# Performance work log

Hardware: AMD Instinct MI355X
Metric: run time of the kernel (lower is better)

The kernel has to match this reference:

```python
import jax, jax.numpy as jnp
import numpy as np

N_HEAD = 16

def setup_inputs() -> dict:
    key = jax.random.key(0)
    ks = jax.random.split(key, 9)
    B, T, C = 4, 2048, 1024
    s = 1.0 / np.sqrt(C)
    return {
        "x":  jax.random.normal(ks[0], (B, T, C), jnp.float32),
        "Wq": jax.random.normal(ks[1], (C, C), jnp.float32) * s,
        "bq": jax.random.normal(ks[2], (C,), jnp.float32) * 0.02,
        "Wk": jax.random.normal(ks[3], (C, C), jnp.float32) * s,
        "bk": jax.random.normal(ks[4], (C,), jnp.float32) * 0.02,
        "Wv": jax.random.normal(ks[5], (C, C), jnp.float32) * s,
        "bv": jax.random.normal(ks[6], (C,), jnp.float32) * 0.02,
        "Wp": jax.random.normal(ks[7], (C, C), jnp.float32) * s,
        "bp": jax.random.normal(ks[8], (C,), jnp.float32) * 0.02,
    }

def reference(x, Wq, bq, Wk, bk, Wv, bv, Wp, bp):
    B, T, C = x.shape
    H, D = N_HEAD, C // N_HEAD
    # torch nn.Linear: y = x @ W^T + b
    q = (x @ Wq.T + bq).reshape(B, T, H, D).transpose(0, 2, 1, 3)  # [B,H,T,D]
    k = (x @ Wk.T + bk).reshape(B, T, H, D).transpose(0, 2, 1, 3)
    v = (x @ Wv.T + bv).reshape(B, T, H, D).transpose(0, 2, 1, 3)
    # full TxT causal attention (non-flash path)
    att = jnp.einsum('bhtd,bhsd->bhts', q, k) * (1.0 / np.sqrt(D))  # [B,H,T,T]
    causal = jnp.tril(jnp.ones((T, T), dtype=bool))
    att = jnp.where(causal[None, None], att, -jnp.inf)
    att = jax.nn.softmax(att, axis=-1)
    y = jnp.einsum('bhts,bhsd->bhtd', att, v)  # [B,H,T,D]
    y = y.transpose(0, 2, 1, 3).reshape(B, T, C)
    return y @ Wp.T + bp
```

## Files before the change

### kernel.cpp

```cpp
#include <hip/hip_runtime.h>

typedef __bf16 bf16_t;
typedef __bf16 bf16x8 __attribute__((ext_vector_type(8)));
typedef __bf16 bf16x4 __attribute__((ext_vector_type(4)));
typedef float f32x4 __attribute__((ext_vector_type(4)));
typedef unsigned short ushort_t;

#define T_SEQ 2048
#define C_DIM 1024
#define NH    16
#define HD    64

__device__ __forceinline__ ushort_t f2bf(float f) {
    unsigned u = __builtin_bit_cast(unsigned, f);
    u += 0x7FFFu + ((u >> 16) & 1u);
    return (ushort_t)(u >> 16);
}

__device__ __forceinline__ void async_cp16(const void* g, void* l) {
    __builtin_amdgcn_global_load_lds(
        (const __attribute__((address_space(1))) void*)g,
        (__attribute__((address_space(3))) void*)l, 16, 0, 0);
}

#define X4  2097152
#define W4  262144
__global__ __launch_bounds__(256)
void cvt_all_kernel(const float* __restrict__ x,  const float* __restrict__ Wq,
                    const float* __restrict__ Wk, const float* __restrict__ Wv,
                    ushort_t* __restrict__ xb,  ushort_t* __restrict__ Wqb,
                    ushort_t* __restrict__ Wkb, ushort_t* __restrict__ Wvb) {
    int i = blockIdx.x * 256 + threadIdx.x;
    const float* src; ushort_t* dst; int off;
    if (i < X4)                { src = x;  dst = xb;  off = i; }
    else if (i < X4 + W4)      { src = Wq; dst = Wqb; off = i - X4; }
    else if (i < X4 + 2 * W4)  { src = Wk; dst = Wkb; off = i - X4 - W4; }
    else                       { src = Wv; dst = Wvb; off = i - X4 - 2 * W4; }
    float4 f = ((const float4*)src)[off];
    ushort4 u;
    u.x = f2bf(f.x); u.y = f2bf(f.y); u.z = f2bf(f.z); u.w = f2bf(f.w);
    ((ushort4*)dst)[off] = u;
}

__global__ __launch_bounds__(256)
void cvt_wp_kernel(const float* __restrict__ Wp, ushort_t* __restrict__ Wpb) {
    int i = blockIdx.x * 256 + threadIdx.x;
    float4 f = ((const float4*)Wp)[i];
    ushort4 u;
    u.x = f2bf(f.x); u.y = f2bf(f.y); u.z = f2bf(f.z); u.w = f2bf(f.w);
    ((ushort4*)Wpb)[i] = u;
}

__device__ __forceinline__ void gemm_core_128(const bf16_t* __restrict__ A,
                                              const bf16_t* __restrict__ B,
                                              f32x4 (&acc)[4][4]) {
    __shared__ alignas(16) ushort_t As[128 * 64];
    __shared__ alignas(16) ushort_t Ws[128 * 64];
    const int tid  = threadIdx.x;
    const int lane = tid & 63;
    const int wv   = tid >> 6;
    const int wm   = wv >> 1, wn = wv & 1;
    const int quad = lane >> 4, ln = lane & 15;
    const int m0 = blockIdx.x * 128, n0 = blockIdx.y * 128;

    f32x4 z4 = {0.f, 0.f, 0.f, 0.f};
#pragma unroll
    for (int i = 0; i < 4; i++)
#pragma unroll
        for (int j = 0; j < 4; j++) acc[i][j] = z4;

    const int lr = lane >> 3;
    const int lc = (lane & 7) ^ lr;
    const bf16_t* Ab = A + (size_t)(m0 + wv * 32 + lr) * 1024 + lc * 8;
    const bf16_t* Bb = B + (size_t)(n0 + wv * 32 + lr) * 1024 + lc * 8;

    for (int kt = 0; kt < 1024; kt += 64) {
#pragma unroll
        for (int p = 0; p < 4; ++p) {
            async_cp16(Ab + (size_t)p * 8192 + kt, &As[(wv * 4 + p) * 512]);
            async_cp16(Bb + (size_t)p * 8192 + kt, &Ws[(wv * 4 + p) * 512]);
        }
        __syncthreads();
#pragma unroll
        for (int ks = 0; ks < 2; ++ks) {
            bf16x8 af[4], bfr[4];
#pragma unroll
            for (int i = 0; i < 4; i++)
                af[i] = *(const bf16x8*)&As[(wm * 64 + i * 16 + ln) * 64 +
                                            (((ks * 4 + quad) ^ (ln & 7)) * 8)];
#pragma unroll
            for (int j = 0; j < 4; j++)
                bfr[j] = *(const bf16x8*)&Ws[(wn * 64 + j * 16 + ln) * 64 +
                                             (((ks * 4 + quad) ^ (ln & 7)) * 8)];
#pragma unroll
            for (int i = 0; i < 4; i++)
#pragma unroll
                for (int j = 0; j < 4; j++)
                    acc[i][j] = __builtin_amdgcn_mfma_f32_16x16x32_bf16(af[i], bfr[j],
                                                                        acc[i][j], 0, 0, 0);
        }
        __syncthreads();
    }
}

__global__ __launch_bounds__(256, 3)
void qkv_gemm_kernel(const bf16_t* __restrict__ xb,
                     const bf16_t* __restrict__ Wqb, const float* __restrict__ bq,
                     const bf16_t* __restrict__ Wkb, const float* __restrict__ bk,
                     const bf16_t* __restrict__ Wvb, const float* __restrict__ bv,
                     ushort_t* __restrict__ Qo, ushort_t* __restrict__ Ko,
                     ushort_t* __restrict__ Vo) {
    const int z = blockIdx.z;
    const bf16_t* W   = (z == 0) ? Wqb : (z == 1) ? Wkb : Wvb;
    const float* bias = (z == 0) ? bq : (z == 1) ? bk : bv;
    ushort_t* outp    = (z == 0) ? Qo : (z == 1) ? Ko : Vo;
    const float fs    = (z == 0) ? 0.18033688011112042f : 1.0f;

    f32x4 acc[4][4];
    gemm_core_128(xb, W, acc);

    const int tid  = threadIdx.x;
    const int lane = tid & 63;
    const int wv2  = tid >> 6;
    const int wm   = wv2 >> 1, wn = wv2 & 1;
    const int quad = lane >> 4, ln = lane & 15;
    const int mbase = blockIdx.x * 128 + wm * 64;
    const int nbase = blockIdx.y * 128 + wn * 64;

#pragma unroll
    for (int j = 0; j < 4; j++) {
        int n = nbase + j * 16 + ln;
        float bj = bias[n];
        int h = n >> 6, d = n & 63;
#pragma unroll
        for (int i = 0; i < 4; i++) {
            int mr = mbase + i * 16 + quad * 4;
            int b = mr >> 11;
            int t = mr & 2047;
            if (z < 2) {
                ushort_t* op = outp + ((size_t)(b * NH + h) * T_SEQ + t) * HD + d;
#pragma unroll
                for (int r = 0; r < 4; r++)
                    op[(size_t)r * HD] = f2bf((acc[i][j][r] + bj) * fs);
            } else {
                ushort4 us;
                us.x = f2bf(acc[i][j][0] + bj);
                us.y = f2bf(acc[i][j][1] + bj);
                us.z = f2bf(acc[i][j][2] + bj);
                us.w = f2bf(acc[i][j][3] + bj);
                *(ushort4*)(outp + ((size_t)(b * NH + h) * HD + d) * T_SEQ + t) = us;
            }
        }
    }
}

__device__ __forceinline__ void qk2_softmax(const ushort_t* __restrict__ Ks,
                                            bf16_t* __restrict__ PsWA,
                                            bf16_t* __restrict__ PsWB,
                                            bf16x8 aqA0, bf16x8 aqA1,
                                            bf16x8 aqB0, bf16x8 aqB1,
                                            bool doA, bool diagA, bool diagB,
                                            int wv, int quad, int ln) {
#pragma unroll
    for (int n16 = 0; n16 < 4; n16++) {
        bf16x8 bk0 = *(const bf16x8*)&Ks[(n16 * 16 + ln) * 72 + quad * 8];
        bf16x8 bk1 = *(const bf16x8*)&Ks[(n16 * 16 + ln) * 72 + 32 + quad * 8];
        f32x4 zB = {0.f, 0.f, 0.f, 0.f};
        zB = __builtin_amdgcn_mfma_f32_16x16x32_bf16(bk0, aqB0, zB, 0, 0, 0);
        zB = __builtin_amdgcn_mfma_f32_16x16x32_bf16(bk1, aqB1, zB, 0, 0, 0);
        if (doA) {
            f32x4 zA = {0.f, 0.f, 0.f, 0.f};
            zA = __builtin_amdgcn_mfma_f32_16x16x32_bf16(bk0, aqA0, zA, 0, 0, 0);
            zA = __builtin_amdgcn_mfma_f32_16x16x32_bf16(bk1, aqA1, zA, 0, 0, 0);
            bf16x4 pa;
#pragma unroll
            for (int r = 0; r < 4; r++) {
                float v = zA[r];
                v = (diagA && (n16 * 16 + quad * 4 + r > wv * 16 + ln)) ? -1e30f : v;
                pa[r] = (bf16_t)__builtin_amdgcn_exp2f(v);
            }
            *(bf16x4*)&PsWA[ln * 72 + n16 * 16 + quad * 4] = pa;
        }
        bf16x4 pb;
#pragma unroll
        for (int r = 0; r < 4; r++) {
            float v = zB[r];
            v = (diagB && (n16 * 16 + quad * 4 + r > wv * 16 + ln)) ? -1e30f : v;
            pb[r] = (bf16_t)__builtin_amdgcn_exp2f(v);
        }
        *(bf16x4*)&PsWB[ln * 72 + n16 * 16 + quad * 4] = pb;
    }
}

__global__ __launch_bounds__(256, 4)
void flash_kernel(const ushort_t* __restrict__ Qw, const ushort_t* __restrict__ Kw,
                  const ushort_t* __restrict__ Vt, ushort_t* __restrict__ Y) {
    __shared__ alignas(16) ushort_t Ks[64 * 72];
    __shared__ alignas(16) ushort_t Vts[64 * 72];
    __shared__ alignas(16) bf16_t PsA[4 * 16 * 72];
    __shared__ alignas(16) bf16_t PsB[4 * 16 * 72];

    const int tid  = threadIdx.x;
    const int lane = tid & 63;
    const int wv   = tid >> 6;
    const int quad = lane >> 4, ln = lane & 15;
    const int L  = blockIdx.y * 16 + blockIdx.x;
    const int m  = L >> 3;
    const int bh = ((m >> 4) << 3) | (L & 7);
    const int p  = m & 15;
    const int qa = p, qb = 31 - p;
    const int b = bh >> 4, h = bh & 15;
    bf16_t* PsWA = &PsA[wv * 1152];
    bf16_t* PsWB = &PsB[wv * 1152];

    bf16x8 ones;
#pragma unroll
    for (int i = 0; i < 8; i++) ones[i] = (bf16_t)1.0f;

    const ushort_t* qpa = Qw + ((size_t)bh * T_SEQ + qa * 64 + wv * 16 + ln) * HD;
    const ushort_t* qpb = Qw + ((size_t)bh * T_SEQ + qb * 64 + wv * 16 + ln) * HD;
    bf16x8 aqA0 = *(const bf16x8*)(qpa + quad * 8);
    bf16x8 aqA1 = *(const bf16x8*)(qpa + 32 + quad * 8);
    bf16x8 aqB0 = *(const bf16x8*)(qpb + quad * 8);
    bf16x8 aqB1 = *(const bf16x8*)(qpb + 32 + quad * 8);

    f32x4 oA[4], oB[4];
    f32x4 z4 = {0.f, 0.f, 0.f, 0.f};
#pragma unroll
    for (int i = 0; i < 4; i++) { oA[i] = z4; oB[i] = z4; }
    f32x4 lA4 = z4, lB4 = z4;

    const int row0 = tid >> 3, c80 = (tid & 7) * 8;
    const int row1 = (256 + tid) >> 3, c81 = c80;

    uint4 pk0, pk1, pv0, pv1;
    pk0 = *(const uint4*)(Kw + ((size_t)bh * T_SEQ + row0) * HD + c80);
    pv0 = *(const uint4*)(Vt + ((size_t)bh * HD + row0) * T_SEQ + c80);
    pk1 = *(const uint4*)(Kw + ((size_t)bh * T_SEQ + row1) * HD + c81);
    pv1 = *(const uint4*)(Vt + ((size_t)bh * HD + row1) * T_SEQ + c81);

    for (int st = 0; st <= qb; ++st) {
        __syncthreads();
        *(uint4*)&Ks[row0 * 72 + c80]  = pk0;
        *(uint4*)&Vts[row0 * 72 + c80] = pv0;
        *(uint4*)&Ks[row1 * 72 + c81]  = pk1;
        *(uint4*)&Vts[row1 * 72 + c81] = pv1;
        if (st < qb) {
            int s1 = (st + 1) * 64;
            pk0 = *(const uint4*)(Kw + ((size_t)bh * T_SEQ + s1 + row0) * HD + c80);
            pv0 = *(const uint4*)(Vt + ((size_t)bh * HD + row0) * T_SEQ + s1 + c80);
            pk1 = *(const uint4*)(Kw + ((size_t)bh * T_SEQ + s1 + row1) * HD + c81);
            pv1 = *(const uint4*)(Vt + ((size_t)bh * HD + row1) * T_SEQ + s1 + c81);
        }
        __syncthreads();

        const bool doA = (st <= qa);
        qk2_softmax(Ks, PsWA, PsWB, aqA0, aqA1, aqB0, aqB1,
                    doA, st == qa, st == qb, wv, quad, ln);

#pragma unroll
        for (int ks = 0; ks < 2; ks++) {
            bf16x8 apA, apB;
            if (doA) {
                apA = *(const bf16x8*)&PsWA[ln * 72 + ks * 32 + quad * 8];
                lA4 = __builtin_amdgcn_mfma_f32_16x16x32_bf16(apA, ones, lA4, 0, 0, 0);
            }
            apB = *(const bf16x8*)&PsWB[ln * 72 + ks * 32 + quad * 8];
            lB4 = __builtin_amdgcn_mfma_f32_16x16x32_bf16(apB, ones, lB4, 0, 0, 0);
#pragma unroll
            for (int d16 = 0; d16 < 4; d16++) {
                bf16x8 bv = *(const bf16x8*)&Vts[(d16 * 16 + ln) * 72 + ks * 32 + quad * 8];
                if (doA)
                    oA[d16] = __builtin_amdgcn_mfma_f32_16x16x32_bf16(apA, bv, oA[d16], 0, 0, 0);
                oB[d16] = __builtin_amdgcn_mfma_f32_16x16x32_bf16(apB, bv, oB[d16], 0, 0, 0);
            }
        }
    }

#pragma unroll
    for (int ph = 0; ph < 2; ph++) {
        f32x4* o = ph ? oB : oA;
        f32x4 l4 = ph ? lB4 : lA4;
        int qt = ph ? qb : qa;
        f32x4 inv = {1.f / l4[0], 1.f / l4[1], 1.f / l4[2], 1.f / l4[3]};
        const int tg = qt * 64 + wv * 16 + quad * 4;
#pragma unroll
        for (int d16 = 0; d16 < 4; d16++) {
#pragma unroll
            for (int r = 0; r < 4; r++) {
                float v = o[d16][r] * inv[r];
                Y[((size_t)b * T_SEQ + tg + r) * C_DIM + h * HD + d16 * 16 + ln] = f2bf(v);
            }
        }
    }
}

__global__ __launch_bounds__(256, 3)
void proj_gemm_kernel(const bf16_t* __restrict__ Yw, const bf16_t* __restrict__ Wpb,
                      const float* __restrict__ bp, float* __restrict__ out) {
    f32x4 acc[4][4];
    gemm_core_128(Yw, Wpb, acc);

    const int tid  = threadIdx.x;
    const int lane = tid & 63;
    const int wv2  = tid >> 6;
    const int wm   = wv2 >> 1, wn = wv2 & 1;
    const int quad = lane >> 4, ln = lane & 15;
    const int mbase = blockIdx.x * 128 + wm * 64;
    const int nbase = blockIdx.y * 128 + wn * 64;

#pragma unroll
    for (int j = 0; j < 4; j++) {
        int n = nbase + j * 16 + ln;
        float bj = bp[n];
#pragma unroll
        for (int i = 0; i < 4; i++) {
            int mr = mbase + i * 16 + quad * 4;
#pragma unroll
            for (int r = 0; r < 4; r++)
                out[(size_t)(mr + r) * C_DIM + n] = acc[i][j][r] + bj;
        }
    }
}

extern "C" void kernel_launch(void* const* d_in, const int* in_sizes, int n_in,
                              void* d_out, int out_size, void* d_ws, size_t ws_size,
                              hipStream_t stream) {
    const float* x  = (const float*)d_in[0];
    const float* Wq = (const float*)d_in[1];
    const float* bq = (const float*)d_in[2];
    const float* Wk = (const float*)d_in[3];
    const float* bk = (const float*)d_in[4];
    const float* Wv = (const float*)d_in[5];
    const float* bv = (const float*)d_in[6];
    const float* Wp = (const float*)d_in[7];
    const float* bp = (const float*)d_in[8];
    float* out = (float*)d_out;

    char* ws = (char*)d_ws;
    const size_t MB = (size_t)1 << 20;
    ushort_t* Qw = (ushort_t*)(ws);
    ushort_t* Kw = (ushort_t*)(ws + 16 * MB);
    ushort_t* Vt = (ushort_t*)(ws + 32 * MB);
    ushort_t* Yw = (ushort_t*)(ws + 48 * MB);
    ushort_t* Wpb = (ushort_t*)(ws);

    ushort_t* xb  = (ushort_t*)out;
    ushort_t* Wqb = (ushort_t*)((char*)out + 16 * MB);
    ushort_t* Wkb = (ushort_t*)((char*)out + 18 * MB);
    ushort_t* Wvb = (ushort_t*)((char*)out + 20 * MB);

    cvt_all_kernel<<<11264, 256, 0, stream>>>(x, Wq, Wk, Wv, xb, Wqb, Wkb, Wvb);

    dim3 g1(64, 8, 3);
    qkv_gemm_kernel<<<g1, 256, 0, stream>>>((const bf16_t*)xb,
                                            (const bf16_t*)Wqb, bq,
                                            (const bf16_t*)Wkb, bk,
                                            (const bf16_t*)Wvb, bv,
                                            Qw, Kw, Vt);

    dim3 g2(16, 64);
    flash_kernel<<<g2, 256, 0, stream>>>(Qw, Kw, Vt, Yw);

    cvt_wp_kernel<<<1024, 256, 0, stream>>>(Wp, Wpb);

    dim3 g3(64, 8, 1);
    proj_gemm_kernel<<<g3, 256, 0, stream>>>((const bf16_t*)Yw, (const bf16_t*)Wpb, bp, out);
}
```

Baseline: 248.4 us.

## Keep softmax probabilities in registers by permuting V layout in LDS

The P tile no longer round-trips through shared memory. The exp outputs of the QK MFMA are placed straight into the A-operand registers of the PV MFMA. For that to work, the key index order inside Vts is permuted (vkpos) when V is stored, so it matches the register layout of the QK accumulator. This removes the LDS writes and reads of P and frees shared memory, at the cost of split 8-byte V stores that may cause more bank conflicts.

```diff
diff --git a/kernel.cpp b/kernel.cpp
--- a/kernel.cpp
+++ b/kernel.cpp
@@ -154,42 +154,8 @@
     }
 }
 
-__device__ __forceinline__ void qk2_softmax(const ushort_t* __restrict__ Ks,
-                                            bf16_t* __restrict__ PsWA,
-                                            bf16_t* __restrict__ PsWB,
-                                            bf16x8 aqA0, bf16x8 aqA1,
-                                            bf16x8 aqB0, bf16x8 aqB1,
-                                            bool doA, bool diagA, bool diagB,
-                                            int wv, int quad, int ln) {
-#pragma unroll
-    for (int n16 = 0; n16 < 4; n16++) {
-        bf16x8 bk0 = *(const bf16x8*)&Ks[(n16 * 16 + ln) * 72 + quad * 8];
-        bf16x8 bk1 = *(const bf16x8*)&Ks[(n16 * 16 + ln) * 72 + 32 + quad * 8];
-        f32x4 zB = {0.f, 0.f, 0.f, 0.f};
-        zB = __builtin_amdgcn_mfma_f32_16x16x32_bf16(bk0, aqB0, zB, 0, 0, 0);
-        zB = __builtin_amdgcn_mfma_f32_16x16x32_bf16(bk1, aqB1, zB, 0, 0, 0);
-        if (doA) {
-            f32x4 zA = {0.f, 0.f, 0.f, 0.f};
-            zA = __builtin_amdgcn_mfma_f32_16x16x32_bf16(bk0, aqA0, zA, 0, 0, 0);
-            zA = __builtin_amdgcn_mfma_f32_16x16x32_bf16(bk1, aqA1, zA, 0, 0, 0);
-            bf16x4 pa;
-#pragma unroll
-            for (int r = 0; r < 4; r++) {
-                float v = zA[r];
-                v = (diagA && (n16 * 16 + quad * 4 + r > wv * 16 + ln)) ? -1e30f : v;
-                pa[r] = (bf16_t)__builtin_amdgcn_exp2f(v);
-            }
-            *(bf16x4*)&PsWA[ln * 72 + n16 * 16 + quad * 4] = pa;
-        }
-        bf16x4 pb;
-#pragma unroll
-        for (int r = 0; r < 4; r++) {
-            float v = zB[r];
-            v = (diagB && (n16 * 16 + quad * 4 + r > wv * 16 + ln)) ? -1e30f : v;
-            pb[r] = (bf16_t)__builtin_amdgcn_exp2f(v);
-        }
-        *(bf16x4*)&PsWB[ln * 72 + n16 * 16 + quad * 4] = pb;
-    }
+__device__ __forceinline__ int vkpos(int s) {
+    return 32 * (s >> 5) + 8 * ((s >> 2) & 3) + 4 * ((s >> 4) & 1) + (s & 3);
 }
 
 __global__ __launch_bounds__(256, 4)
@@ -197,8 +163,6 @@
                   const ushort_t* __restrict__ Vt, ushort_t* __restrict__ Y) {
     __shared__ alignas(16) ushort_t Ks[64 * 72];
     __shared__ alignas(16) ushort_t Vts[64 * 72];
-    __shared__ alignas(16) bf16_t PsA[4 * 16 * 72];
-    __shared__ alignas(16) bf16_t PsB[4 * 16 * 72];
 
     const int tid  = threadIdx.x;
     const int lane = tid & 63;
@@ -210,8 +174,6 @@
     const int p  = m & 15;
     const int qa = p, qb = 31 - p;
     const int b = bh >> 4, h = bh & 15;
-    bf16_t* PsWA = &PsA[wv * 1152];
-    bf16_t* PsWB = &PsB[wv * 1152];
 
     bf16x8 ones;
 #pragma unroll
@@ -231,48 +193,81 @@
     f32x4 lA4 = z4, lB4 = z4;
 
     const int row0 = tid >> 3, c80 = (tid & 7) * 8;
-    const int row1 = (256 + tid) >> 3, c81 = c80;
+    const int row1 = (256 + tid) >> 3;
+    const int kp0 = vkpos(c80);
+    const int kp1 = vkpos(c80 + 4);
 
     uint4 pk0, pk1, pv0, pv1;
     pk0 = *(const uint4*)(Kw + ((size_t)bh * T_SEQ + row0) * HD + c80);
     pv0 = *(const uint4*)(Vt + ((size_t)bh * HD + row0) * T_SEQ + c80);
-    pk1 = *(const uint4*)(Kw + ((size_t)bh * T_SEQ + row1) * HD + c81);
-    pv1 = *(const uint4*)(Vt + ((size_t)bh * HD + row1) * T_SEQ + c81);
+    pk1 = *(const uint4*)(Kw + ((size_t)bh * T_SEQ + row1) * HD + c80);
+    pv1 = *(const uint4*)(Vt + ((size_t)bh * HD + row1) * T_SEQ + c80);
+
+    const int qrow = wv * 16 + ln;
 
     for (int st = 0; st <= qb; ++st) {
         __syncthreads();
-        *(uint4*)&Ks[row0 * 72 + c80]  = pk0;
-        *(uint4*)&Vts[row0 * 72 + c80] = pv0;
-        *(uint4*)&Ks[row1 * 72 + c81]  = pk1;
-        *(uint4*)&Vts[row1 * 72 + c81] = pv1;
+        *(uint4*)&Ks[row0 * 72 + c80] = pk0;
+        *(uint4*)&Ks[row1 * 72 + c80] = pk1;
+        {
+            uint2 a0 = {pv0.x, pv0.y}, a1 = {pv0.z, pv0.w};
+            uint2 b0 = {pv1.x, pv1.y}, b1 = {pv1.z, pv1.w};
+            *(uint2*)&Vts[row0 * 72 + kp0] = a0;
+            *(uint2*)&Vts[row0 * 72 + kp1] = a1;
+            *(uint2*)&Vts[row1 * 72 + kp0] = b0;
+            *(uint2*)&Vts[row1 * 72 + kp1] = b1;
+        }
         if (st < qb) {
             int s1 = (st + 1) * 64;
             pk0 = *(const uint4*)(Kw + ((size_t)bh * T_SEQ + s1 + row0) * HD + c80);
             pv0 = *(const uint4*)(Vt + ((size_t)bh * HD + row0) * T_SEQ + s1 + c80);
-            pk1 = *(const uint4*)(Kw + ((size_t)bh * T_SEQ + s1 + row1) * HD + c81);
-            pv1 = *(const uint4*)(Vt + ((size_t)bh * HD + row1) * T_SEQ + s1 + c81);
+            pk1 = *(const uint4*)(Kw + ((size_t)bh * T_SEQ + s1 + row1) * HD + c80);
+            pv1 = *(const uint4*)(Vt + ((size_t)bh * HD + row1) * T_SEQ + s1 + c80);
         }
         __syncthreads();
 
         const bool doA = (st <= qa);
-        qk2_softmax(Ks, PsWA, PsWB, aqA0, aqA1, aqB0, aqB1,
-                    doA, st == qa, st == qb, wv, quad, ln);
+        const bool dgA = (st == qa), dgB = (st == qb);
+
+        bf16x8 apA[2], apB[2];
+#pragma unroll
+        for (int n16 = 0; n16 < 4; n16++) {
+            bf16x8 bk0 = *(const bf16x8*)&Ks[(n16 * 16 + ln) * 72 + quad * 8];
+            bf16x8 bk1 = *(const bf16x8*)&Ks[(n16 * 16 + ln) * 72 + 32 + quad * 8];
+            const int ks = n16 >> 1, hf = (n16 & 1) * 4;
+            f32x4 zB = {0.f, 0.f, 0.f, 0.f};
+            zB = __builtin_amdgcn_mfma_f32_16x16x32_bf16(bk0, aqB0, zB, 0, 0, 0);
+            zB = __builtin_amdgcn_mfma_f32_16x16x32_bf16(bk1, aqB1, zB, 0, 0, 0);
+            if (doA) {
+                f32x4 zA = {0.f, 0.f, 0.f, 0.f};
+                zA = __builtin_amdgcn_mfma_f32_16x16x32_bf16(bk0, aqA0, zA, 0, 0, 0);
+                zA = __builtin_amdgcn_mfma_f32_16x16x32_bf16(bk1, aqA1, zA, 0, 0, 0);
+#pragma unroll
+                for (int r = 0; r < 4; r++) {
+                    float v = zA[r];
+                    v = (dgA && (n16 * 16 + quad * 4 + r > qrow)) ? -1e30f : v;
+                    apA[ks][hf + r] = (bf16_t)__builtin_amdgcn_exp2f(v);
+                }
+            }
+#pragma unroll
+            for (int r = 0; r < 4; r++) {
+                float v = zB[r];
+                v = (dgB && (n16 * 16 + quad * 4 + r > qrow)) ? -1e30f : v;
+                apB[ks][hf + r] = (bf16_t)__builtin_amdgcn_exp2f(v);
+            }
+        }
 
 #pragma unroll
         for (int ks = 0; ks < 2; ks++) {
-            bf16x8 apA, apB;
-            if (doA) {
-                apA = *(const bf16x8*)&PsWA[ln * 72 + ks * 32 + quad * 8];
-                lA4 = __builtin_amdgcn_mfma_f32_16x16x32_bf16(apA, ones, lA4, 0, 0, 0);
-            }
-            apB = *(const bf16x8*)&PsWB[ln * 72 + ks * 32 + quad * 8];
-            lB4 = __builtin_amdgcn_mfma_f32_16x16x32_bf16(apB, ones, lB4, 0, 0, 0);
+            if (doA)
+                lA4 = __builtin_amdgcn_mfma_f32_16x16x32_bf16(apA[ks], ones, lA4, 0, 0, 0);
+            lB4 = __builtin_amdgcn_mfma_f32_16x16x32_bf16(apB[ks], ones, lB4, 0, 0, 0);
 #pragma unroll
             for (int d16 = 0; d16 < 4; d16++) {
                 bf16x8 bv = *(const bf16x8*)&Vts[(d16 * 16 + ln) * 72 + ks * 32 + quad * 8];
                 if (doA)
-                    oA[d16] = __builtin_amdgcn_mfma_f32_16x16x32_bf16(apA, bv, oA[d16], 0, 0, 0);
-                oB[d16] = __builtin_amdgcn_mfma_f32_16x16x32_bf16(apB, bv, oB[d16], 0, 0, 0);
+                    oA[d16] = __builtin_amdgcn_mfma_f32_16x16x32_bf16(apA[ks], bv, oA[d16], 0, 0, 0);
+                oB[d16] = __builtin_amdgcn_mfma_f32_16x16x32_bf16(apB[ks], bv, oB[d16], 0, 0, 0);
             }
         }
     }
```

After: 239.9 us. -3.4%, faster.
